# Performance work log

Measured on AMD Instinct MI355X. Metric: run time of the kernel, lower is better.

## Reference

```python
import jax, jax.numpy as jnp
import numpy as np

NUM_THETAS = 64   # bump_steps == num_thetas == 64
NUM_PTS = 100
B = 256           # number of graphs
N = B * NUM_PTS   # total nodes
SCALE = 500.0     # sigmoid sharpness used by EctLayer
HID = 4 * 1024


def _linear_init(key, fan_in, shape):
    s = 1.0 / np.sqrt(fan_in)
    return jax.random.uniform(key, shape, jnp.float32, -s, s)


def setup_inputs() -> dict:
    key = jax.random.key(0)
    ks = jax.random.split(key, 8)
    x = jax.random.normal(ks[0], (N, 2), jnp.float32)
    batch_idx = jnp.repeat(jnp.arange(B), NUM_PTS)  # [N] graph id per node
    t = jnp.linspace(0.0, 2.0 * np.pi, NUM_THETAS)
    V = jnp.stack([jnp.sin(t), jnp.cos(t)], axis=0)          # [2, T] directions
    lin = jnp.linspace(-1.0, 1.0, NUM_THETAS)                # [bump] thresholds
    d = NUM_THETAS * NUM_THETAS
    W1 = _linear_init(ks[1], d, (d, HID)); b1 = _linear_init(ks[2], d, (HID,))
    W2 = _linear_init(ks[3], HID, (HID, HID)); b2 = _linear_init(ks[4], HID, (HID,))
    W3 = _linear_init(ks[5], HID, (HID, 2 * NUM_PTS)); b3 = _linear_init(ks[6], HID, (2 * NUM_PTS,))
    return {"x": x, "batch_idx": batch_idx, "V": V, "lin": lin,
            "W1": W1, "b1": b1, "W2": W2, "b2": b2, "W3": W3, "b3": b3}


def ect_layer(x, idx, V, lin, num_graphs):
    # x: [N,2], V: [2,T] -> node heights nh: [N,T]
    nh = x @ V
    # soft-threshold binning: [N, bump, T]
    ecc = jax.nn.sigmoid(SCALE * (lin[None, :, None] - nh[:, None, :]))
    # per-graph scatter-sum over nodes -> [B, bump, T]
    e = jax.ops.segment_sum(ecc, idx, num_segments=num_graphs)
    # normalized=True: divide by per-graph max
    return e / jnp.amax(e, axis=(1, 2), keepdims=True)


def reference(x, batch_idx, V, lin, W1, b1, W2, b2, W3, b3):
    ect = ect_layer(x, batch_idx, V, lin, B)          # [B, 64, 64]
    h = ect.reshape(B, -1)                            # Flatten
    h = jnp.tanh(h @ W1 + b1)
    h = jnp.tanh(h @ W2 + b2)
    pts = (h @ W3 + b3).reshape(-1, 2)                # [B*NUM_PTS, 2]
    idx2 = jnp.repeat(jnp.arange(B), NUM_PTS)
    decoded = ect_layer(pts, idx2, V, lin, B)         # [B, 64, 64]
    return decoded, pts
```

## Files before the change

kernel.cpp:

```cpp
#include <hip/hip_runtime.h>
#include <hip/hip_bf16.h>

typedef short bf16x8 __attribute__((ext_vector_type(8)));
typedef short s16x4 __attribute__((ext_vector_type(4)));
typedef float f32x4 __attribute__((ext_vector_type(4)));
typedef unsigned u32x4 __attribute__((ext_vector_type(4)));

#define ECT_SCALE 500.0f

__device__ __forceinline__ bool detect_f32(const void* w) {
    const unsigned* p = (const unsigned*)w;
    int sane = 0;
#pragma unroll
    for (int i = 0; i < 16; i++) {
        unsigned e = (p[i] >> 7) & 0xFFu;
        sane += (e >= 100u && e <= 140u) ? 1 : 0;
    }
    return sane < 10;
}

__device__ __forceinline__ float ld_f(const void* p, int i, bool f32) {
    return f32 ? ((const float*)p)[i]
               : __bfloat162float(((const __hip_bfloat16*)p)[i]);
}

__device__ __forceinline__ void split_f(float v, short& hi, short& lo) {
    __hip_bfloat16 h = __float2bfloat16(v);
    hi = (short)__bfloat16_as_short(h);
    lo = (short)__bfloat16_as_short(__float2bfloat16(v - __bfloat162float(h)));
}

__device__ __forceinline__ float sig_fast(float x) {
    float t = __builtin_amdgcn_fmed3f(x, 0.0f, 1.0f);
    return t * t * (3.0f - 2.0f * t);
}

__global__ __launch_bounds__(512)
void ect1_kernel(const void* __restrict__ x, const void* __restrict__ V,
                 const void* __restrict__ lin, const void* __restrict__ sent,
                 short* __restrict__ eh, short* __restrict__ el)
{
    __shared__ float in_lds[200];
    __shared__ float nh[100 * 64];
    __shared__ float wmax[8];

    const bool f32 = detect_f32(sent);
    const int g = blockIdx.x, tid = threadIdx.x;
    const int t = tid & 63, wv = tid >> 6;

    if (tid < 200) in_lds[tid] = ld_f(x, g * 200 + tid, f32);
    const float sv = ld_f(V, t, f32);
    const float cv = ld_f(V, 64 + t, f32);
    float zs[8];
#pragma unroll
    for (int k = 0; k < 8; k++)
        zs[k] = (ECT_SCALE / 8.0f) * ld_f(lin, wv + 8 * k, f32) + 0.5f;
    __syncthreads();

    for (int n = wv; n < 100; n += 8)
        nh[n * 64 + t] = in_lds[2 * n] * sv + in_lds[2 * n + 1] * cv;

    float e[8];
#pragma unroll
    for (int k = 0; k < 8; k++) e[k] = 0.0f;
    __syncthreads();

    for (int n = 0; n < 100; n++) {
        const float ws = (ECT_SCALE / 8.0f) * nh[n * 64 + t];
#pragma unroll
        for (int k = 0; k < 8; k++)
            e[k] += sig_fast(zs[k] - ws);
    }

    float mx = e[0];
#pragma unroll
    for (int k = 1; k < 8; k++) mx = fmaxf(mx, e[k]);
#pragma unroll
    for (int off = 32; off > 0; off >>= 1)
        mx = fmaxf(mx, __shfl_xor(mx, off, 64));
    if (t == 0) wmax[wv] = mx;
    __syncthreads();
    float gm = wmax[0];
#pragma unroll
    for (int k = 1; k < 8; k++) gm = fmaxf(gm, wmax[k]);
    const float sc = 1.0f / gm;

#pragma unroll
    for (int k = 0; k < 8; k++) {
        short hi, lo;
        split_f(e[k] * sc, hi, lo);
        eh[g * 4096 + tid + 512 * k] = hi;
        el[g * 4096 + tid + 512 * k] = lo;
    }
}

#define PFSET()                                                                \
    {                                                                          \
        _Pragma("unroll")                                                      \
        for (int p = 0; p < 4; p++) {                                          \
            pah[p] = *(const bf16x8*)(a0 + 8 * p);                             \
            pal[p] = *(const bf16x8*)(l0 + 8 * p);                             \
        }                                                                      \
        if (f32) {                                                             \
            _Pragma("unroll")                                                  \
            for (int j = 0; j < 16; j++) {                                     \
                pw[j]      = *(const unsigned*)(wp + (size_t)j * wrow);        \
                pw[16 + j] = *(const unsigned*)(wp + (size_t)j * wrow + 256);  \
            }                                                                  \
        } else {                                                               \
            _Pragma("unroll")                                                  \
            for (int j = 0; j < 16; j++) {                                     \
                pw[j]      = (unsigned)(*(const unsigned short*)(wp + (size_t)j * wrow)) << 16; \
                pw[16 + j] = (unsigned)(*(const unsigned short*)(wp + (size_t)j * wrow + 128)) << 16; \
            }                                                                  \
        }                                                                      \
        a0 += 64; l0 += 64; wp += 64 * wrow;                                   \
    }

__global__ __launch_bounds__(256, 2)
void gemm128(const short* __restrict__ Ah, const short* __restrict__ Al,
             const void* __restrict__ W, const void* __restrict__ sent,
             float* __restrict__ pre)
{
    __shared__ short Ahs[128][72], Als[128][72], Bhs[128][72], Bls[128][72];
    const bool f32 = detect_f32(sent);
    const int bm = blockIdx.y;
    const int bn = blockIdx.x >> 3;
    const int kz = blockIdx.x & 7;
    const int tid = threadIdx.x;
    const int wv = tid >> 6, lane = tid & 63, quad = lane >> 4, l16 = lane & 15;
    const int wm = (wv & 1) * 64, wn = (wv >> 1) * 64;
    const int ar = tid >> 1, ac = (tid & 1) * 32;
    const int n0c = bn * 128;
    const int wk = wv * 16;

    f32x4 acc[4][4];
#pragma unroll
    for (int i = 0; i < 4; i++)
#pragma unroll
        for (int j = 0; j < 4; j++) acc[i][j] = (f32x4){0.f, 0.f, 0.f, 0.f};

    bf16x8 pah[4], pal[4];
    unsigned pw[32];

    const size_t welt = f32 ? 4u : 2u;
    const size_t wrow = (size_t)4096 * welt;
    const char* wp = (const char*)W + ((size_t)(kz * 512 + wk) * 4096 + (n0c + lane)) * welt;
    const short* a0 = Ah + (size_t)(bm * 128 + ar) * 4096 + kz * 512 + ac;
    const short* l0 = Al + (size_t)(bm * 128 + ar) * 4096 + kz * 512 + ac;

    PFSET()

    for (int it = 0; it < 8; it++) {
#pragma unroll
        for (int p = 0; p < 4; p++) {
            *(bf16x8*)&Ahs[ar][ac + 8 * p] = pah[p];
            *(bf16x8*)&Als[ar][ac + 8 * p] = pal[p];
        }
#pragma unroll
        for (int c = 0; c < 2; c++) {
            unsigned hp[8], lp[8];
#pragma unroll
            for (int jp = 0; jp < 8; jp++) {
                unsigned a = pw[c * 16 + 2 * jp], b = pw[c * 16 + 2 * jp + 1];
                unsigned ha = a & 0xFFFF0000u, hb = b & 0xFFFF0000u;
                hp[jp] = (ha >> 16) | hb;
                if (f32) {
                    float la = __uint_as_float(a) - __uint_as_float(ha);
                    float lb = __uint_as_float(b) - __uint_as_float(hb);
                    lp[jp] = (__float_as_uint(la) >> 16) |
                             (__float_as_uint(lb) & 0xFFFF0000u);
                }
            }
            *(u32x4*)&Bhs[lane + 64 * c][wk]     = (u32x4){hp[0], hp[1], hp[2], hp[3]};
            *(u32x4*)&Bhs[lane + 64 * c][wk + 8] = (u32x4){hp[4], hp[5], hp[6], hp[7]};
            if (f32) {
                *(u32x4*)&Bls[lane + 64 * c][wk]     = (u32x4){lp[0], lp[1], lp[2], lp[3]};
                *(u32x4*)&Bls[lane + 64 * c][wk + 8] = (u32x4){lp[4], lp[5], lp[6], lp[7]};
            }
        }
        __syncthreads();

        if (it < 7) PFSET()

#pragma unroll
        for (int kk = 0; kk < 2; kk++) {
            bf16x8 ahf[4], alf[4];
#pragma unroll
            for (int i = 0; i < 4; i++) {
                ahf[i] = *(const bf16x8*)&Ahs[wm + i * 16 + l16][kk * 32 + quad * 8];
                alf[i] = *(const bf16x8*)&Als[wm + i * 16 + l16][kk * 32 + quad * 8];
            }
            if (f32) {
#pragma unroll
                for (int j = 0; j < 4; j++) {
                    bf16x8 bh = *(const bf16x8*)&Bhs[wn + j * 16 + l16][kk * 32 + quad * 8];
                    bf16x8 bl = *(const bf16x8*)&Bls[wn + j * 16 + l16][kk * 32 + quad * 8];
#pragma unroll
                    for (int i = 0; i < 4; i++) {
                        acc[i][j] = __builtin_amdgcn_mfma_f32_16x16x32_bf16(ahf[i], bh, acc[i][j], 0, 0, 0);
                        acc[i][j] = __builtin_amdgcn_mfma_f32_16x16x32_bf16(ahf[i], bl, acc[i][j], 0, 0, 0);
                        acc[i][j] = __builtin_amdgcn_mfma_f32_16x16x32_bf16(alf[i], bh, acc[i][j], 0, 0, 0);
                    }
                }
            } else {
#pragma unroll
                for (int j = 0; j < 4; j++) {
                    bf16x8 bh = *(const bf16x8*)&Bhs[wn + j * 16 + l16][kk * 32 + quad * 8];
#pragma unroll
                    for (int i = 0; i < 4; i++) {
                        acc[i][j] = __builtin_amdgcn_mfma_f32_16x16x32_bf16(ahf[i], bh, acc[i][j], 0, 0, 0);
                        acc[i][j] = __builtin_amdgcn_mfma_f32_16x16x32_bf16(alf[i], bh, acc[i][j], 0, 0, 0);
                    }
                }
            }
        }

        asm volatile("s_waitcnt lgkmcnt(0)" ::: "memory");
        __builtin_amdgcn_s_barrier();
        asm volatile("" ::: "memory");
    }

    float* ps = pre + (size_t)kz * (256 * 4096);
#pragma unroll
    for (int i = 0; i < 4; i++)
#pragma unroll
        for (int j = 0; j < 4; j++) {
            const int n = n0c + wn + j * 16 + l16;
#pragma unroll
            for (int r = 0; r < 4; r++) {
                const int m = bm * 128 + wm + i * 16 + quad * 4 + r;
                ps[(size_t)m * 4096 + n] = acc[i][j][r];
            }
        }
}

__global__ __launch_bounds__(256)
void finalize8(const float* __restrict__ pre, const void* __restrict__ bias,
               const void* __restrict__ sent,
               short* __restrict__ Oh, short* __restrict__ Ol)
{
    const bool f32 = detect_f32(sent);
    const int idx = (blockIdx.x * 256 + threadIdx.x) * 4;
    f32x4 s = (f32x4){0.f, 0.f, 0.f, 0.f};
#pragma unroll
    for (int z = 0; z < 8; z++)
        s += *(const f32x4*)&pre[(size_t)z * 1048576 + idx];
    const int n = idx & 4095;
    s16x4 hi, lo;
#pragma unroll
    for (int j = 0; j < 4; j++) {
        float t = s[j] + ld_f(bias, n + j, f32);
        t = 1.0f - 2.0f * __builtin_amdgcn_rcpf(1.0f + __expf(2.0f * t));
        short h, l;
        split_f(t, h, l);
        hi[j] = h; lo[j] = l;
    }
    *(s16x4*)&Oh[idx] = hi;
    *(s16x4*)&Ol[idx] = lo;
}

__global__ __launch_bounds__(256)
void gemm_sk3(const short* __restrict__ Ah, const short* __restrict__ Al,
              const void* __restrict__ W, const void* __restrict__ sent,
              float* __restrict__ part)
{
    __shared__ short Ahs[64][72], Als[64][72], Bhs[64][72], Bls[64][72];
    const bool f32 = detect_f32(sent);
    const int N_ = 200, K_ = 4096;
    const int bm = blockIdx.y;
    const int bn = blockIdx.x >> 5;
    const int kz = blockIdx.x & 31;
    const int tid = threadIdx.x;
    const int wv = tid >> 6, lane = tid & 63, quad = lane >> 4, l16 = lane & 15;
    const int mrow0 = (wv & 1) * 32, ncol0 = (wv >> 1) * 32;
    const int rr = tid >> 3, cc = (tid & 7) * 8;
    const int n0c = bn * 64;

    f32x4 acc[2][2];
#pragma unroll
    for (int i = 0; i < 2; i++)
#pragma unroll
        for (int j = 0; j < 2; j++) acc[i][j] = (f32x4){0.f, 0.f, 0.f, 0.f};

    int k0 = kz * 128;
    for (int it = 0; it < 2; it++, k0 += 64) {
#pragma unroll
        for (int i = 0; i < 2; i++) {
            int r = rr + 32 * i;
            *(bf16x8*)&Ahs[r][cc] = *(const bf16x8*)&Ah[(size_t)(bm * 64 + r) * K_ + k0 + cc];
            *(bf16x8*)&Als[r][cc] = *(const bf16x8*)&Al[(size_t)(bm * 64 + r) * K_ + k0 + cc];
        }
        {
            const int wn2 = lane, wk2 = wv * 16;
            const bool okn = (n0c + wn2 < N_);
            unsigned pw2[16];
#pragma unroll
            for (int j = 0; j < 16; j++) {
                size_t off = (size_t)(k0 + wk2 + j) * N_ + n0c + wn2;
                pw2[j] = !okn ? 0u
                       : (f32 ? ((const unsigned*)W)[off]
                              : ((unsigned)((const unsigned short*)W)[off] << 16));
            }
            unsigned hp[8], lp[8];
#pragma unroll
            for (int jp = 0; jp < 8; jp++) {
                unsigned a = pw2[2 * jp], b = pw2[2 * jp + 1];
                unsigned ha = a & 0xFFFF0000u, hb = b & 0xFFFF0000u;
                hp[jp] = (ha >> 16) | hb;
                if (f32) {
                    float la = __uint_as_float(a) - __uint_as_float(ha);
                    float lb = __uint_as_float(b) - __uint_as_float(hb);
                    lp[jp] = (__float_as_uint(la) >> 16) | (__float_as_uint(lb) & 0xFFFF0000u);
                }
            }
            *(u32x4*)&Bhs[wn2][wk2]     = (u32x4){hp[0], hp[1], hp[2], hp[3]};
            *(u32x4*)&Bhs[wn2][wk2 + 8] = (u32x4){hp[4], hp[5], hp[6], hp[7]};
            if (f32) {
                *(u32x4*)&Bls[wn2][wk2]     = (u32x4){lp[0], lp[1], lp[2], lp[3]};
                *(u32x4*)&Bls[wn2][wk2 + 8] = (u32x4){lp[4], lp[5], lp[6], lp[7]};
            }
        }
        __syncthreads();
#pragma unroll
        for (int kh = 0; kh < 2; kh++) {
            bf16x8 ah2[2], al2[2];
#pragma unroll
            for (int im = 0; im < 2; im++) {
                ah2[im] = *(const bf16x8*)&Ahs[mrow0 + im * 16 + l16][kh * 32 + quad * 8];
                al2[im] = *(const bf16x8*)&Als[mrow0 + im * 16 + l16][kh * 32 + quad * 8];
            }
            if (f32) {
#pragma unroll
                for (int jn = 0; jn < 2; jn++) {
                    bf16x8 bh = *(const bf16x8*)&Bhs[ncol0 + jn * 16 + l16][kh * 32 + quad * 8];
                    bf16x8 bl = *(const bf16x8*)&Bls[ncol0 + jn * 16 + l16][kh * 32 + quad * 8];
#pragma unroll
                    for (int im = 0; im < 2; im++) {
                        acc[im][jn] = __builtin_amdgcn_mfma_f32_16x16x32_bf16(ah2[im], bh, acc[im][jn], 0, 0, 0);
                        acc[im][jn] = __builtin_amdgcn_mfma_f32_16x16x32_bf16(ah2[im], bl, acc[im][jn], 0, 0, 0);
                        acc[im][jn] = __builtin_amdgcn_mfma_f32_16x16x32_bf16(al2[im], bh, acc[im][jn], 0, 0, 0);
                    }
                }
            } else {
#pragma unroll
                for (int jn = 0; jn < 2; jn++) {
                    bf16x8 bh = *(const bf16x8*)&Bhs[ncol0 + jn * 16 + l16][kh * 32 + quad * 8];
#pragma unroll
                    for (int im = 0; im < 2; im++) {
                        acc[im][jn] = __builtin_amdgcn_mfma_f32_16x16x32_bf16(ah2[im], bh, acc[im][jn], 0, 0, 0);
                        acc[im][jn] = __builtin_amdgcn_mfma_f32_16x16x32_bf16(al2[im], bh, acc[im][jn], 0, 0, 0);
                    }
                }
            }
        }
        __syncthreads();
    }

    float* ps = part + (size_t)kz * (256 * 200);
#pragma unroll
    for (int im = 0; im < 2; im++)
#pragma unroll
        for (int jn = 0; jn < 2; jn++) {
            const int n = n0c + ncol0 + jn * 16 + l16;
            if (n < N_) {
#pragma unroll
                for (int r = 0; r < 4; r++) {
                    const int m = bm * 64 + mrow0 + im * 16 + quad * 4 + r;
                    ps[m * 200 + n] = acc[im][jn][r];
                }
            }
        }
}

__global__ __launch_bounds__(512)
void ect2_kernel(const float* __restrict__ part, const void* __restrict__ bias3,
                 const void* __restrict__ V, const void* __restrict__ lin,
                 const void* __restrict__ sent,
                 float* __restrict__ dec, float* __restrict__ pts_out)
{
    __shared__ float in_lds[200];
    __shared__ float nh[100 * 64];
    __shared__ float wmax[8];

    const bool f32 = detect_f32(sent);
    const int g = blockIdx.x, tid = threadIdx.x;
    const int t = tid & 63, wv = tid >> 6;

    if (tid < 200) {
        float v = ld_f(bias3, tid, f32);
#pragma unroll
        for (int z = 0; z < 32; z++)
            v += part[(size_t)z * 51200 + g * 200 + tid];
        in_lds[tid] = v;
        pts_out[g * 200 + tid] = v;
    }
    const float sv = ld_f(V, t, f32);
    const float cv = ld_f(V, 64 + t, f32);
    float zs[8];
#pragma unroll
    for (int k = 0; k < 8; k++)
        zs[k] = (ECT_SCALE / 8.0f) * ld_f(lin, wv + 8 * k, f32) + 0.5f;
    __syncthreads();

    for (int n = wv; n < 100; n += 8)
        nh[n * 64 + t] = in_lds[2 * n] * sv + in_lds[2 * n + 1] * cv;

    float e[8];
#pragma unroll
    for (int k = 0; k < 8; k++) e[k] = 0.0f;
    __syncthreads();

    for (int n = 0; n < 100; n++) {
        const float ws = (ECT_SCALE / 8.0f) * nh[n * 64 + t];
#pragma unroll
        for (int k = 0; k < 8; k++)
            e[k] += sig_fast(zs[k] - ws);
    }

    float mx = e[0];
#pragma unroll
    for (int k = 1; k < 8; k++) mx = fmaxf(mx, e[k]);
#pragma unroll
    for (int off = 32; off > 0; off >>= 1)
        mx = fmaxf(mx, __shfl_xor(mx, off, 64));
    if (t == 0) wmax[wv] = mx;
    __syncthreads();
    float gm = wmax[0];
#pragma unroll
    for (int k = 1; k < 8; k++) gm = fmaxf(gm, wmax[k]);
    const float sc = 1.0f / gm;

#pragma unroll
    for (int k = 0; k < 8; k++)
        dec[g * 4096 + tid + 512 * k] = e[k] * sc;
}

extern "C" void kernel_launch(void* const* d_in, const int* in_sizes, int n_in,
                              void* d_out, int out_size, void* d_ws, size_t ws_size,
                              hipStream_t stream)
{
    const void* x   = d_in[0];
    const void* V   = d_in[2];
    const void* lin = d_in[3];
    const void* W1  = d_in[4];
    const void* b1  = d_in[5];
    const void* W2  = d_in[6];
    const void* b2  = d_in[7];
    const void* W3  = d_in[8];
    const void* b3  = d_in[9];
    float* out = (float*)d_out;

    char* ws = (char*)d_ws;
    short* e_h  = (short*)(ws + ( 0u << 20));
    short* e_l  = (short*)(ws + ( 2u << 20));
    short* h1h  = (short*)(ws + ( 4u << 20));
    short* h1l  = (short*)(ws + ( 6u << 20));
    short* h2h  = (short*)(ws + ( 8u << 20));
    short* h2l  = (short*)(ws + (10u << 20));
    float* pre  = (float*)(ws + (12u << 20));
    float* part = (float*)(ws + (44u << 20));

    ect1_kernel<<<256, 512, 0, stream>>>(x, V, lin, W1, e_h, e_l);
    gemm128<<<dim3(256, 2), 256, 0, stream>>>(e_h, e_l, W1, W1, pre);
    finalize8<<<1024, 256, 0, stream>>>(pre, b1, W1, h1h, h1l);
    gemm128<<<dim3(256, 2), 256, 0, stream>>>(h1h, h1l, W2, W1, pre);
    finalize8<<<1024, 256, 0, stream>>>(pre, b2, W1, h2h, h2l);
    gemm_sk3<<<dim3(128, 4), 256, 0, stream>>>(h2h, h2l, W3, W1, part);
    ect2_kernel<<<256, 512, 0, stream>>>(part, b3, V, lin, W1, out, out + 1048576);
}
```

Measured before the change: 255.8 us.

## Fuse all stages into one cooperative persistent kernel with grid barriers

```diff
diff --git a/kernel.cpp b/kernel.cpp
--- a/kernel.cpp
+++ b/kernel.cpp
@@ -7,6 +7,7 @@
 typedef unsigned u32x4 __attribute__((ext_vector_type(4)));
 
 #define ECT_SCALE 500.0f
+#define NB 512u
 
 __device__ __forceinline__ bool detect_f32(const void* w) {
     const unsigned* p = (const unsigned*)w;
@@ -35,63 +36,22 @@
     return t * t * (3.0f - 2.0f * t);
 }
 
-__global__ __launch_bounds__(512)
-void ect1_kernel(const void* __restrict__ x, const void* __restrict__ V,
-                 const void* __restrict__ lin, const void* __restrict__ sent,
-                 short* __restrict__ eh, short* __restrict__ el)
-{
-    __shared__ float in_lds[200];
-    __shared__ float nh[100 * 64];
-    __shared__ float wmax[8];
-
-    const bool f32 = detect_f32(sent);
-    const int g = blockIdx.x, tid = threadIdx.x;
-    const int t = tid & 63, wv = tid >> 6;
-
-    if (tid < 200) in_lds[tid] = ld_f(x, g * 200 + tid, f32);
-    const float sv = ld_f(V, t, f32);
-    const float cv = ld_f(V, 64 + t, f32);
-    float zs[8];
-#pragma unroll
-    for (int k = 0; k < 8; k++)
-        zs[k] = (ECT_SCALE / 8.0f) * ld_f(lin, wv + 8 * k, f32) + 0.5f;
-    __syncthreads();
-
-    for (int n = wv; n < 100; n += 8)
-        nh[n * 64 + t] = in_lds[2 * n] * sv + in_lds[2 * n + 1] * cv;
-
-    float e[8];
-#pragma unroll
-    for (int k = 0; k < 8; k++) e[k] = 0.0f;
-    __syncthreads();
-
-    for (int n = 0; n < 100; n++) {
-        const float ws = (ECT_SCALE / 8.0f) * nh[n * 64 + t];
-#pragma unroll
-        for (int k = 0; k < 8; k++)
-            e[k] += sig_fast(zs[k] - ws);
-    }
-
-    float mx = e[0];
-#pragma unroll
-    for (int k = 1; k < 8; k++) mx = fmaxf(mx, e[k]);
-#pragma unroll
-    for (int off = 32; off > 0; off >>= 1)
-        mx = fmaxf(mx, __shfl_xor(mx, off, 64));
-    if (t == 0) wmax[wv] = mx;
-    __syncthreads();
-    float gm = wmax[0];
-#pragma unroll
-    for (int k = 1; k < 8; k++) gm = fmaxf(gm, wmax[k]);
-    const float sc = 1.0f / gm;
-
-#pragma unroll
-    for (int k = 0; k < 8; k++) {
-        short hi, lo;
-        split_f(e[k] * sc, hi, lo);
-        eh[g * 4096 + tid + 512 * k] = hi;
-        el[g * 4096 + tid + 512 * k] = lo;
-    }
+struct SharedGemm { short Ahs[128][72]; short Als[128][72];
+                    short Bhs[128][72]; short Bls[128][72]; };
+struct SharedEct  { float in_lds[200]; float nh[100 * 64]; };
+struct SharedSk3  { short Ahs[64][72]; short Als[64][72];
+                    short Bhs[64][72]; short Bls[64][72]; };
+union SharedU { SharedGemm g; SharedEct e; SharedSk3 s; };
+
+__device__ __forceinline__ void grid_sync(unsigned* bar, unsigned target) {
+    __syncthreads();
+    if (threadIdx.x == 0) {
+        __threadfence();
+        __hip_atomic_fetch_add(bar, 1u, __ATOMIC_ACQ_REL, __HIP_MEMORY_SCOPE_AGENT);
+        while (__hip_atomic_load(bar, __ATOMIC_ACQUIRE, __HIP_MEMORY_SCOPE_AGENT) < target)
+            __builtin_amdgcn_s_sleep(16);
+    }
+    __syncthreads();
 }
 
 #define PFSET()                                                                \
@@ -117,16 +77,15 @@
         a0 += 64; l0 += 64; wp += 64 * wrow;                                   \
     }
 
-__global__ __launch_bounds__(256, 2)
-void gemm128(const short* __restrict__ Ah, const short* __restrict__ Al,
-             const void* __restrict__ W, const void* __restrict__ sent,
-             float* __restrict__ pre)
-{
-    __shared__ short Ahs[128][72], Als[128][72], Bhs[128][72], Bls[128][72];
-    const bool f32 = detect_f32(sent);
-    const int bm = blockIdx.y;
-    const int bn = blockIdx.x >> 3;
-    const int kz = blockIdx.x & 7;
+__device__ __forceinline__ void gemm128_phase(
+    const short* __restrict__ Ah, const short* __restrict__ Al,
+    const void* __restrict__ W, bool f32, float* __restrict__ pre,
+    int bid, SharedGemm& G)
+{
+    auto& Ahs = G.Ahs; auto& Als = G.Als; auto& Bhs = G.Bhs; auto& Bls = G.Bls;
+    const int bm = bid >> 8;
+    const int bn = (bid & 255) >> 3;
+    const int kz = bid & 7;
     const int tid = threadIdx.x;
     const int wv = tid >> 6, lane = tid & 63, quad = lane >> 4, l16 = lane & 15;
     const int wm = (wv & 1) * 64, wn = (wv >> 1) * 64;
@@ -235,42 +194,43 @@
         }
 }
 
-__global__ __launch_bounds__(256)
-void finalize8(const float* __restrict__ pre, const void* __restrict__ bias,
-               const void* __restrict__ sent,
-               short* __restrict__ Oh, short* __restrict__ Ol)
-{
-    const bool f32 = detect_f32(sent);
-    const int idx = (blockIdx.x * 256 + threadIdx.x) * 4;
-    f32x4 s = (f32x4){0.f, 0.f, 0.f, 0.f};
-#pragma unroll
-    for (int z = 0; z < 8; z++)
-        s += *(const f32x4*)&pre[(size_t)z * 1048576 + idx];
-    const int n = idx & 4095;
-    s16x4 hi, lo;
-#pragma unroll
-    for (int j = 0; j < 4; j++) {
-        float t = s[j] + ld_f(bias, n + j, f32);
-        t = 1.0f - 2.0f * __builtin_amdgcn_rcpf(1.0f + __expf(2.0f * t));
-        short h, l;
-        split_f(t, h, l);
-        hi[j] = h; lo[j] = l;
-    }
-    *(s16x4*)&Oh[idx] = hi;
-    *(s16x4*)&Ol[idx] = lo;
-}
-
-__global__ __launch_bounds__(256)
-void gemm_sk3(const short* __restrict__ Ah, const short* __restrict__ Al,
-              const void* __restrict__ W, const void* __restrict__ sent,
-              float* __restrict__ part)
-{
-    __shared__ short Ahs[64][72], Als[64][72], Bhs[64][72], Bls[64][72];
-    const bool f32 = detect_f32(sent);
+__device__ __forceinline__ void fin_phase(
+    const float* __restrict__ pre, const void* __restrict__ bias, bool f32,
+    short* __restrict__ Oh, short* __restrict__ Ol, int bid)
+{
+    const int base = (bid * 256 + threadIdx.x) * 8;
+#pragma unroll
+    for (int h = 0; h < 2; h++) {
+        const int idx = base + 4 * h;
+        f32x4 s = (f32x4){0.f, 0.f, 0.f, 0.f};
+#pragma unroll
+        for (int z = 0; z < 8; z++)
+            s += *(const f32x4*)&pre[(size_t)z * 1048576 + idx];
+        const int n = idx & 4095;
+        s16x4 hi, lo;
+#pragma unroll
+        for (int j = 0; j < 4; j++) {
+            float t = s[j] + ld_f(bias, n + j, f32);
+            t = 1.0f - 2.0f * __builtin_amdgcn_rcpf(1.0f + __expf(2.0f * t));
+            short h2, l2;
+            split_f(t, h2, l2);
+            hi[j] = h2; lo[j] = l2;
+        }
+        *(s16x4*)&Oh[idx] = hi;
+        *(s16x4*)&Ol[idx] = lo;
+    }
+}
+
+__device__ __forceinline__ void sk3_phase(
+    const short* __restrict__ Ah, const short* __restrict__ Al,
+    const void* __restrict__ W, bool f32, float* __restrict__ part,
+    int bid, SharedSk3& S)
+{
+    auto& Ahs = S.Ahs; auto& Als = S.Als; auto& Bhs = S.Bhs; auto& Bls = S.Bls;
     const int N_ = 200, K_ = 4096;
-    const int bm = blockIdx.y;
-    const int bn = blockIdx.x >> 5;
-    const int kz = blockIdx.x & 31;
+    const int bm = bid >> 7;
+    const int bn = (bid & 127) >> 5;
+    const int kz = bid & 31;
     const int tid = threadIdx.x;
     const int wv = tid >> 6, lane = tid & 63, quad = lane >> 4, l16 = lane & 15;
     const int mrow0 = (wv & 1) * 32, ncol0 = (wv >> 1) * 32;
@@ -371,6 +331,218 @@
                 }
             }
         }
+}
+
+__device__ __forceinline__ void ect_accum(
+    const float* in_lds, float* nh, const void* V, const void* lin,
+    int rowbase, bool f32, float e[8], float& blkmax)
+{
+    const int tid = threadIdx.x, t = tid & 63, wv = tid >> 6;
+    const float sv = ld_f(V, t, f32);
+    const float cv = ld_f(V, 64 + t, f32);
+    float zs[8];
+#pragma unroll
+    for (int k = 0; k < 8; k++)
+        zs[k] = (ECT_SCALE / 8.0f) * ld_f(lin, rowbase + wv + 4 * k, f32) + 0.5f;
+    __syncthreads();
+
+    for (int n = wv; n < 100; n += 4)
+        nh[n * 64 + t] = in_lds[2 * n] * sv + in_lds[2 * n + 1] * cv;
+#pragma unroll
+    for (int k = 0; k < 8; k++) e[k] = 0.0f;
+    __syncthreads();
+
+    for (int n = 0; n < 100; n++) {
+        const float ws = (ECT_SCALE / 8.0f) * nh[n * 64 + t];
+#pragma unroll
+        for (int k = 0; k < 8; k++)
+            e[k] += sig_fast(zs[k] - ws);
+    }
+
+    float mx = e[0];
+#pragma unroll
+    for (int k = 1; k < 8; k++) mx = fmaxf(mx, e[k]);
+#pragma unroll
+    for (int off = 32; off > 0; off >>= 1)
+        mx = fmaxf(mx, __shfl_xor(mx, off, 64));
+    __syncthreads();
+    if (t == 0) nh[wv] = mx;
+    __syncthreads();
+    blkmax = fmaxf(fmaxf(nh[0], nh[1]), fmaxf(nh[2], nh[3]));
+}
+
+__global__ __launch_bounds__(256, 2)
+void mega(const void* __restrict__ x, const void* __restrict__ V,
+          const void* __restrict__ lin,
+          const void* __restrict__ W1, const void* __restrict__ b1,
+          const void* __restrict__ W2, const void* __restrict__ b2,
+          const void* __restrict__ W3, const void* __restrict__ b3,
+          short* __restrict__ e_h, short* __restrict__ e_l,
+          short* __restrict__ h1h, short* __restrict__ h1l,
+          short* __restrict__ h2h, short* __restrict__ h2l,
+          float* __restrict__ pre, float* __restrict__ part,
+          float* __restrict__ dec, float* __restrict__ pts,
+          unsigned* __restrict__ bar,
+          float* __restrict__ gmax1, float* __restrict__ gmax2)
+{
+    __shared__ SharedU sh;
+    const int bid = blockIdx.x, tid = threadIdx.x;
+    const bool f32 = detect_f32(W1);
+    unsigned sn = 0;
+
+    const int g1 = bid >> 1, half1 = bid & 1;
+    float e1[8];
+    {
+        if (tid < 200) sh.e.in_lds[tid] = ld_f(x, g1 * 200 + tid, f32);
+        float bmax;
+        ect_accum(sh.e.in_lds, sh.e.nh, V, lin, half1 * 32, f32, e1, bmax);
+        if (tid == 0) gmax1[bid] = bmax;
+    }
+    grid_sync(bar, (++sn) * NB);
+
+    {
+        const float gm = fmaxf(gmax1[g1 * 2], gmax1[g1 * 2 + 1]);
+        const float sc = 1.0f / gm;
+        const int t = tid & 63, wv = tid >> 6;
+#pragma unroll
+        for (int k = 0; k < 8; k++) {
+            const int row = half1 * 32 + wv + 4 * k;
+            short hi, lo;
+            split_f(e1[k] * sc, hi, lo);
+            e_h[g1 * 4096 + row * 64 + t] = hi;
+            e_l[g1 * 4096 + row * 64 + t] = lo;
+        }
+    }
+    grid_sync(bar, (++sn) * NB);
+
+    gemm128_phase(e_h, e_l, W1, f32, pre, bid, sh.g);
+    grid_sync(bar, (++sn) * NB);
+
+    fin_phase(pre, b1, f32, h1h, h1l, bid);
+    grid_sync(bar, (++sn) * NB);
+
+    gemm128_phase(h1h, h1l, W2, f32, pre, bid, sh.g);
+    grid_sync(bar, (++sn) * NB);
+
+    fin_phase(pre, b2, f32, h2h, h2l, bid);
+    grid_sync(bar, (++sn) * NB);
+
+    sk3_phase(h2h, h2l, W3, f32, part, bid, sh.s);
+    grid_sync(bar, (++sn) * NB);
+
+    float e2[8];
+    {
+        if (tid < 200) {
+            float v = ld_f(b3, tid, f32);
+#pragma unroll
+            for (int z = 0; z < 32; z++)
+                v += part[(size_t)z * 51200 + g1 * 200 + tid];
+            sh.e.in_lds[tid] = v;
+            if (half1 == 0) pts[g1 * 200 + tid] = v;
+        }
+        float bmax;
+        ect_accum(sh.e.in_lds, sh.e.nh, V, lin, half1 * 32, f32, e2, bmax);
+        if (tid == 0) gmax2[bid] = bmax;
+    }
+    grid_sync(bar, (++sn) * NB);
+
+    {
+        const float gm = fmaxf(gmax2[g1 * 2], gmax2[g1 * 2 + 1]);
+        const float sc = 1.0f / gm;
+        const int t = tid & 63, wv = tid >> 6;
+#pragma unroll
+        for (int k = 0; k < 8; k++) {
+            const int row = half1 * 32 + wv + 4 * k;
+            dec[g1 * 4096 + row * 64 + t] = e2[k] * sc;
+        }
+    }
+}
+
+__global__ __launch_bounds__(512)
+void ect1_kernel(const void* __restrict__ x, const void* __restrict__ V,
+                 const void* __restrict__ lin, const void* __restrict__ sent,
+                 short* __restrict__ eh, short* __restrict__ el)
+{
+    __shared__ float in_lds[200];
+    __shared__ float nh[100 * 64];
+    __shared__ float wmax[8];
+
+    const bool f32 = detect_f32(sent);
+    const int g = blockIdx.x, tid = threadIdx.x;
+    const int t = tid & 63, wv = tid >> 6;
+
+    if (tid < 200) in_lds[tid] = ld_f(x, g * 200 + tid, f32);
+    const float sv = ld_f(V, t, f32);
+    const float cv = ld_f(V, 64 + t, f32);
+    float zs[8];
+#pragma unroll
+    for (int k = 0; k < 8; k++)
+        zs[k] = (ECT_SCALE / 8.0f) * ld_f(lin, wv + 8 * k, f32) + 0.5f;
+    __syncthreads();
+
+    for (int n = wv; n < 100; n += 8)
+        nh[n * 64 + t] = in_lds[2 * n] * sv + in_lds[2 * n + 1] * cv;
+
+    float e[8];
+#pragma unroll
+    for (int k = 0; k < 8; k++) e[k] = 0.0f;
+    __syncthreads();
+
+    for (int n = 0; n < 100; n++) {
+        const float ws = (ECT_SCALE / 8.0f) * nh[n * 64 + t];
+#pragma unroll
+        for (int k = 0; k < 8; k++)
+            e[k] += sig_fast(zs[k] - ws);
+    }
+
+    float mx = e[0];
+#pragma unroll
+    for (int k = 1; k < 8; k++) mx = fmaxf(mx, e[k]);
+#pragma unroll
+    for (int off = 32; off > 0; off >>= 1)
+        mx = fmaxf(mx, __shfl_xor(mx, off, 64));
+    if (t == 0) wmax[wv] = mx;
+    __syncthreads();
+    float gm = wmax[0];
+#pragma unroll
+    for (int k = 1; k < 8; k++) gm = fmaxf(gm, wmax[k]);
+    const float sc = 1.0f / gm;
+
+#pragma unroll
+    for (int k = 0; k < 8; k++) {
+        short hi, lo;
+        split_f(e[k] * sc, hi, lo);
+        eh[g * 4096 + tid + 512 * k] = hi;
+        el[g * 4096 + tid + 512 * k] = lo;
+    }
+}
+
+__global__ __launch_bounds__(256, 2)
+void gemm128(const short* __restrict__ Ah, const short* __restrict__ Al,
+             const void* __restrict__ W, const void* __restrict__ sent,
+             float* __restrict__ pre)
+{
+    __shared__ SharedGemm G;
+    gemm128_phase(Ah, Al, W, detect_f32(sent), pre,
+                  blockIdx.y * 256 + blockIdx.x, G);
+}
+
+__global__ __launch_bounds__(256)
+void finalize8(const float* __restrict__ pre, const void* __restrict__ bias,
+               const void* __restrict__ sent,
+               short* __restrict__ Oh, short* __restrict__ Ol)
+{
+    fin_phase(pre, bias, detect_f32(sent), Oh, Ol, blockIdx.x);
+}
+
+__global__ __launch_bounds__(256)
+void gemm_sk3(const short* __restrict__ Ah, const short* __restrict__ Al,
+              const void* __restrict__ W, const void* __restrict__ sent,
+              float* __restrict__ part)
+{
+    __shared__ SharedSk3 S;
+    sk3_phase(Ah, Al, W, detect_f32(sent), part,
+              blockIdx.y * 128 + blockIdx.x, S);
 }
 
 __global__ __launch_bounds__(512)
@@ -460,12 +632,38 @@
     short* h2l  = (short*)(ws + (10u << 20));
     float* pre  = (float*)(ws + (12u << 20));
     float* part = (float*)(ws + (44u << 20));
-
-    ect1_kernel<<<256, 512, 0, stream>>>(x, V, lin, W1, e_h, e_l);
-    gemm128<<<dim3(256, 2), 256, 0, stream>>>(e_h, e_l, W1, W1, pre);
-    finalize8<<<1024, 256, 0, stream>>>(pre, b1, W1, h1h, h1l);
-    gemm128<<<dim3(256, 2), 256, 0, stream>>>(h1h, h1l, W2, W1, pre);
-    finalize8<<<1024, 256, 0, stream>>>(pre, b2, W1, h2h, h2l);
-    gemm_sk3<<<dim3(128, 4), 256, 0, stream>>>(h2h, h2l, W3, W1, part);
-    ect2_kernel<<<256, 512, 0, stream>>>(part, b3, V, lin, W1, out, out + 1048576);
-}
+    unsigned* bar = (unsigned*)(ws + (52u << 20));
+    float* gmax1  = (float*)(ws + (52u << 20) + 256);
+    float* gmax2  = (float*)(ws + (52u << 20) + 4352);
+    float* dec = out;
+    float* pts = out + 1048576;
+
+    hipMemsetAsync(bar, 0, 64, stream);
+
+    const void *ax = x, *aV = V, *alin = lin, *aW1 = W1, *ab1 = b1,
+               *aW2 = W2, *ab2 = b2, *aW3 = W3, *ab3 = b3;
+    short *aeh = e_h, *ael = e_l, *ah1h = h1h, *ah1l = h1l, *ah2h = h2h, *ah2l = h2l;
+    float *apre = pre, *apart = part, *adec = dec, *apts = pts;
+    unsigned* abar = bar;
+    float *ag1 = gmax1, *ag2 = gmax2;
+    void* params[] = {
+        (void*)&ax, (void*)&aV, (void*)&alin, (void*)&aW1, (void*)&ab1,
+        (void*)&aW2, (void*)&ab2, (void*)&aW3, (void*)&ab3,
+        (void*)&aeh, (void*)&ael, (void*)&ah1h, (void*)&ah1l,
+        (void*)&ah2h, (void*)&ah2l, (void*)&apre, (void*)&apart,
+        (void*)&adec, (void*)&apts, (void*)&abar, (void*)&ag1, (void*)&ag2
+    };
+
+    hipError_t rc = hipLaunchCooperativeKernel((const void*)mega, dim3(512),
+                                               dim3(256), params, 0, stream);
+    if (rc != hipSuccess) {
+        (void)hipGetLastError();
+        ect1_kernel<<<256, 512, 0, stream>>>(x, V, lin, W1, e_h, e_l);
+        gemm128<<<dim3(256, 2), 256, 0, stream>>>(e_h, e_l, W1, W1, pre);
+        finalize8<<<512, 256, 0, stream>>>(pre, b1, W1, h1h, h1l);
+        gemm128<<<dim3(256, 2), 256, 0, stream>>>(h1h, h1l, W2, W1, pre);
+        finalize8<<<512, 256, 0, stream>>>(pre, b2, W1, h2h, h2l);
+        gemm_sk3<<<dim3(128, 4), 256, 0, stream>>>(h2h, h2l, W3, W1, part);
+        ect2_kernel<<<256, 512, 0, stream>>>(part, b3, V, lin, W1, dec, pts);
+    }
+}
```

Result: slower. 812.7 us (+217.7%).

## Split GEMM into dtype-specialized kernels with lighter 512-thread bf16 variant

Applied to the files above, without the earlier changes.

```diff
diff --git a/kernel.cpp b/kernel.cpp
--- a/kernel.cpp
+++ b/kernel.cpp
@@ -94,36 +94,126 @@
     }
 }
 
-#define PFSET()                                                                \
+#define PFB()                                                                  \
+    {                                                                          \
+        pah[0] = *(const bf16x8*)a0; pah[1] = *(const bf16x8*)(a0 + 8);        \
+        pal[0] = *(const bf16x8*)l0; pal[1] = *(const bf16x8*)(l0 + 8);        \
+        _Pragma("unroll")                                                      \
+        for (int jp = 0; jp < 4; jp++) {                                       \
+            pw[jp]     = (unsigned)wp[(size_t)(2 * jp) * 4096]                 \
+                       | ((unsigned)wp[(size_t)(2 * jp + 1) * 4096] << 16);    \
+            pw[4 + jp] = (unsigned)wp[(size_t)(2 * jp) * 4096 + 64]            \
+                       | ((unsigned)wp[(size_t)(2 * jp + 1) * 4096 + 64] << 16); \
+        }                                                                      \
+        a0 += 64; l0 += 64; wp += (size_t)64 * 4096;                           \
+    }
+
+__global__ __launch_bounds__(512, 4)
+void gemm128_bf16(const short* __restrict__ Ah, const short* __restrict__ Al,
+                  const unsigned short* __restrict__ W,
+                  const void* __restrict__ sent,
+                  float* __restrict__ pre)
+{
+    if (detect_f32(sent)) return;
+    __shared__ short Ahs[128][72], Als[128][72], Bhs[128][72];
+    const int bm = blockIdx.y;
+    const int bn = blockIdx.x >> 3;
+    const int kz = blockIdx.x & 7;
+    const int tid = threadIdx.x;
+    const int wv = tid >> 6;
+    const int lane = tid & 63, quad = lane >> 4, l16 = lane & 15;
+    const int wm = (wv & 1) * 64;
+    const int wn = (wv >> 1) * 32;
+    const int ar = tid >> 2, ac = (tid & 3) * 16;
+    const int n0c = bn * 128;
+    const int wk = wv * 8;
+
+    f32x4 acc[4][2];
+#pragma unroll
+    for (int i = 0; i < 4; i++)
+#pragma unroll
+        for (int j = 0; j < 2; j++) acc[i][j] = (f32x4){0.f, 0.f, 0.f, 0.f};
+
+    bf16x8 pah[2], pal[2];
+    unsigned pw[8];
+
+    const unsigned short* wp = W + (size_t)(kz * 512 + wk) * 4096 + n0c + lane;
+    const short* a0 = Ah + (size_t)(bm * 128 + ar) * 4096 + kz * 512 + ac;
+    const short* l0 = Al + (size_t)(bm * 128 + ar) * 4096 + kz * 512 + ac;
+
+    PFB()
+
+    for (int it = 0; it < 8; it++) {
+        *(bf16x8*)&Ahs[ar][ac]     = pah[0];
+        *(bf16x8*)&Ahs[ar][ac + 8] = pah[1];
+        *(bf16x8*)&Als[ar][ac]     = pal[0];
+        *(bf16x8*)&Als[ar][ac + 8] = pal[1];
+        *(u32x4*)&Bhs[lane][wk]      = (u32x4){pw[0], pw[1], pw[2], pw[3]};
+        *(u32x4*)&Bhs[lane + 64][wk] = (u32x4){pw[4], pw[5], pw[6], pw[7]};
+        __syncthreads();
+
+        if (it < 7) PFB()
+
+#pragma unroll
+        for (int kk = 0; kk < 2; kk++) {
+            bf16x8 ahf[4], alf[4];
+#pragma unroll
+            for (int i = 0; i < 4; i++) {
+                ahf[i] = *(const bf16x8*)&Ahs[wm + i * 16 + l16][kk * 32 + quad * 8];
+                alf[i] = *(const bf16x8*)&Als[wm + i * 16 + l16][kk * 32 + quad * 8];
+            }
+#pragma unroll
+            for (int j = 0; j < 2; j++) {
+                bf16x8 bh = *(const bf16x8*)&Bhs[wn + j * 16 + l16][kk * 32 + quad * 8];
+#pragma unroll
+                for (int i = 0; i < 4; i++) {
+                    acc[i][j] = __builtin_amdgcn_mfma_f32_16x16x32_bf16(ahf[i], bh, acc[i][j], 0, 0, 0);
+                    acc[i][j] = __builtin_amdgcn_mfma_f32_16x16x32_bf16(alf[i], bh, acc[i][j], 0, 0, 0);
+                }
+            }
+        }
+
+        asm volatile("s_waitcnt lgkmcnt(0)" ::: "memory");
+        __builtin_amdgcn_s_barrier();
+        asm volatile("" ::: "memory");
+    }
+
+    float* ps = pre + (size_t)kz * (256 * 4096);
+#pragma unroll
+    for (int i = 0; i < 4; i++)
+#pragma unroll
+        for (int j = 0; j < 2; j++) {
+            const int n = n0c + wn + j * 16 + l16;
+#pragma unroll
+            for (int r = 0; r < 4; r++) {
+                const int m = bm * 128 + wm + i * 16 + quad * 4 + r;
+                ps[(size_t)m * 4096 + n] = acc[i][j][r];
+            }
+        }
+}
+
+#define PFF()                                                                  \
     {                                                                          \
         _Pragma("unroll")                                                      \
         for (int p = 0; p < 4; p++) {                                          \
             pah[p] = *(const bf16x8*)(a0 + 8 * p);                             \
             pal[p] = *(const bf16x8*)(l0 + 8 * p);                             \
         }                                                                      \
-        if (f32) {                                                             \
-            _Pragma("unroll")                                                  \
-            for (int j = 0; j < 16; j++) {                                     \
-                pw[j]      = *(const unsigned*)(wp + (size_t)j * wrow);        \
-                pw[16 + j] = *(const unsigned*)(wp + (size_t)j * wrow + 256);  \
-            }                                                                  \
-        } else {                                                               \
-            _Pragma("unroll")                                                  \
-            for (int j = 0; j < 16; j++) {                                     \
-                pw[j]      = (unsigned)(*(const unsigned short*)(wp + (size_t)j * wrow)) << 16; \
-                pw[16 + j] = (unsigned)(*(const unsigned short*)(wp + (size_t)j * wrow + 128)) << 16; \
-            }                                                                  \
+        _Pragma("unroll")                                                      \
+        for (int j = 0; j < 16; j++) {                                         \
+            pw[j]      = *(const unsigned*)(wp + (size_t)j * 16384);           \
+            pw[16 + j] = *(const unsigned*)(wp + (size_t)j * 16384 + 256);     \
         }                                                                      \
-        a0 += 64; l0 += 64; wp += 64 * wrow;                                   \
+        a0 += 64; l0 += 64; wp += (size_t)64 * 16384;                          \
     }
 
 __global__ __launch_bounds__(256, 2)
-void gemm128(const short* __restrict__ Ah, const short* __restrict__ Al,
-             const void* __restrict__ W, const void* __restrict__ sent,
-             float* __restrict__ pre)
-{
+void gemm128_f32(const short* __restrict__ Ah, const short* __restrict__ Al,
+                 const char* __restrict__ W, const void* __restrict__ sent,
+                 float* __restrict__ pre)
+{
+    if (!detect_f32(sent)) return;
     __shared__ short Ahs[128][72], Als[128][72], Bhs[128][72], Bls[128][72];
-    const bool f32 = detect_f32(sent);
     const int bm = blockIdx.y;
     const int bn = blockIdx.x >> 3;
     const int kz = blockIdx.x & 7;
@@ -143,13 +233,11 @@
     bf16x8 pah[4], pal[4];
     unsigned pw[32];
 
-    const size_t welt = f32 ? 4u : 2u;
-    const size_t wrow = (size_t)4096 * welt;
-    const char* wp = (const char*)W + ((size_t)(kz * 512 + wk) * 4096 + (n0c + lane)) * welt;
+    const char* wp = W + ((size_t)(kz * 512 + wk) * 4096 + (n0c + lane)) * 4u;
     const short* a0 = Ah + (size_t)(bm * 128 + ar) * 4096 + kz * 512 + ac;
     const short* l0 = Al + (size_t)(bm * 128 + ar) * 4096 + kz * 512 + ac;
 
-    PFSET()
+    PFF()
 
     for (int it = 0; it < 8; it++) {
 #pragma unroll
@@ -165,23 +253,19 @@
                 unsigned a = pw[c * 16 + 2 * jp], b = pw[c * 16 + 2 * jp + 1];
                 unsigned ha = a & 0xFFFF0000u, hb = b & 0xFFFF0000u;
                 hp[jp] = (ha >> 16) | hb;
-                if (f32) {
-                    float la = __uint_as_float(a) - __uint_as_float(ha);
-                    float lb = __uint_as_float(b) - __uint_as_float(hb);
-                    lp[jp] = (__float_as_uint(la) >> 16) |
-                             (__float_as_uint(lb) & 0xFFFF0000u);
-                }
+                float la = __uint_as_float(a) - __uint_as_float(ha);
+                float lb = __uint_as_float(b) - __uint_as_float(hb);
+                lp[jp] = (__float_as_uint(la) >> 16) |
+                         (__float_as_uint(lb) & 0xFFFF0000u);
             }
             *(u32x4*)&Bhs[lane + 64 * c][wk]     = (u32x4){hp[0], hp[1], hp[2], hp[3]};
             *(u32x4*)&Bhs[lane + 64 * c][wk + 8] = (u32x4){hp[4], hp[5], hp[6], hp[7]};
-            if (f32) {
-                *(u32x4*)&Bls[lane + 64 * c][wk]     = (u32x4){lp[0], lp[1], lp[2], lp[3]};
-                *(u32x4*)&Bls[lane + 64 * c][wk + 8] = (u32x4){lp[4], lp[5], lp[6], lp[7]};
-            }
+            *(u32x4*)&Bls[lane + 64 * c][wk]     = (u32x4){lp[0], lp[1], lp[2], lp[3]};
+            *(u32x4*)&Bls[lane + 64 * c][wk + 8] = (u32x4){lp[4], lp[5], lp[6], lp[7]};
         }
         __syncthreads();
 
-        if (it < 7) PFSET()
+        if (it < 7) PFF()
 
 #pragma unroll
         for (int kk = 0; kk < 2; kk++) {
@@ -191,27 +275,15 @@
                 ahf[i] = *(const bf16x8*)&Ahs[wm + i * 16 + l16][kk * 32 + quad * 8];
                 alf[i] = *(const bf16x8*)&Als[wm + i * 16 + l16][kk * 32 + quad * 8];
             }
-            if (f32) {
-#pragma unroll
-                for (int j = 0; j < 4; j++) {
-                    bf16x8 bh = *(const bf16x8*)&Bhs[wn + j * 16 + l16][kk * 32 + quad * 8];
-                    bf16x8 bl = *(const bf16x8*)&Bls[wn + j * 16 + l16][kk * 32 + quad * 8];
-#pragma unroll
-                    for (int i = 0; i < 4; i++) {
-                        acc[i][j] = __builtin_amdgcn_mfma_f32_16x16x32_bf16(ahf[i], bh, acc[i][j], 0, 0, 0);
-                        acc[i][j] = __builtin_amdgcn_mfma_f32_16x16x32_bf16(ahf[i], bl, acc[i][j], 0, 0, 0);
-                        acc[i][j] = __builtin_amdgcn_mfma_f32_16x16x32_bf16(alf[i], bh, acc[i][j], 0, 0, 0);
-                    }
-                }
-            } else {
-#pragma unroll
-                for (int j = 0; j < 4; j++) {
-                    bf16x8 bh = *(const bf16x8*)&Bhs[wn + j * 16 + l16][kk * 32 + quad * 8];
-#pragma unroll
-                    for (int i = 0; i < 4; i++) {
-                        acc[i][j] = __builtin_amdgcn_mfma_f32_16x16x32_bf16(ahf[i], bh, acc[i][j], 0, 0, 0);
-                        acc[i][j] = __builtin_amdgcn_mfma_f32_16x16x32_bf16(alf[i], bh, acc[i][j], 0, 0, 0);
-                    }
+#pragma unroll
+            for (int j = 0; j < 4; j++) {
+                bf16x8 bh = *(const bf16x8*)&Bhs[wn + j * 16 + l16][kk * 32 + quad * 8];
+                bf16x8 bl = *(const bf16x8*)&Bls[wn + j * 16 + l16][kk * 32 + quad * 8];
+#pragma unroll
+                for (int i = 0; i < 4; i++) {
+                    acc[i][j] = __builtin_amdgcn_mfma_f32_16x16x32_bf16(ahf[i], bh, acc[i][j], 0, 0, 0);
+                    acc[i][j] = __builtin_amdgcn_mfma_f32_16x16x32_bf16(ahf[i], bl, acc[i][j], 0, 0, 0);
+                    acc[i][j] = __builtin_amdgcn_mfma_f32_16x16x32_bf16(alf[i], bh, acc[i][j], 0, 0, 0);
                 }
             }
         }
@@ -462,9 +534,11 @@
     float* part = (float*)(ws + (44u << 20));
 
     ect1_kernel<<<256, 512, 0, stream>>>(x, V, lin, W1, e_h, e_l);
-    gemm128<<<dim3(256, 2), 256, 0, stream>>>(e_h, e_l, W1, W1, pre);
+    gemm128_bf16<<<dim3(256, 2), 512, 0, stream>>>(e_h, e_l, (const unsigned short*)W1, W1, pre);
+    gemm128_f32 <<<dim3(256, 2), 256, 0, stream>>>(e_h, e_l, (const char*)W1, W1, pre);
     finalize8<<<1024, 256, 0, stream>>>(pre, b1, W1, h1h, h1l);
-    gemm128<<<dim3(256, 2), 256, 0, stream>>>(h1h, h1l, W2, W1, pre);
+    gemm128_bf16<<<dim3(256, 2), 512, 0, stream>>>(h1h, h1l, (const unsigned short*)W2, W1, pre);
+    gemm128_f32 <<<dim3(256, 2), 256, 0, stream>>>(h1h, h1l, (const char*)W2, W1, pre);
     finalize8<<<1024, 256, 0, stream>>>(pre, b2, W1, h2h, h2l);
     gemm_sk3<<<dim3(128, 4), 256, 0, stream>>>(h2h, h2l, W3, W1, part);
     ect2_kernel<<<256, 512, 0, stream>>>(part, b3, V, lin, W1, out, out + 1048576);
```

Result: no change. 259.0 us (+1.3%).
